# Kernel optimization log

Measured on AMD Instinct MI355X. Metric: run time of the kernel, lower is better.

## Reference

```python
import jax, jax.numpy as jnp
import numpy as np

# Block sizes: 3-hop sampled bipartite graphs (src -> dst per layer)
N_SRC0, N_DST0, E0 = 500_000, 100_000, 1_000_000
N_DST1, E1 = 10_000, 100_000
N_DST2, E2 = 1_024, 10_240
D_IN, D_HID, N_CLS = 128, 128, 47


def setup_inputs() -> dict:
    key = jax.random.key(0)
    ks = jax.random.split(key, 16)
    feats = jax.random.normal(ks[0], (N_SRC0, D_IN), dtype=jnp.float32)
    src0 = jax.random.randint(ks[1], (E0,), 0, N_SRC0)
    dst0 = jax.random.randint(ks[2], (E0,), 0, N_DST0)
    src1 = jax.random.randint(ks[3], (E1,), 0, N_DST0)
    dst1 = jax.random.randint(ks[4], (E1,), 0, N_DST1)
    src2 = jax.random.randint(ks[5], (E2,), 0, N_DST1)
    dst2 = jax.random.randint(ks[6], (E2,), 0, N_DST2)
    # fsi.inverse_idx reindex + NPFeatureShuffle all-to-all -> two permutations
    inverse_idx = jax.random.permutation(ks[7], N_DST0)
    shuffle_idx = jax.random.permutation(ks[8], N_DST0)
    def glorot(k, fan_in, fan_out):
        lim = np.sqrt(6.0 / (fan_in + fan_out)).astype(np.float32)
        return jax.random.uniform(k, (fan_in, fan_out), jnp.float32, -lim, lim)
    W0 = glorot(ks[9], D_IN, D_HID)
    b0 = jnp.zeros((D_HID,), jnp.float32)
    W1 = glorot(ks[10], D_HID, D_HID)
    b1 = jnp.zeros((D_HID,), jnp.float32)
    W2 = glorot(ks[11], D_HID, N_CLS)
    b2 = jnp.zeros((N_CLS,), jnp.float32)
    return dict(feats=feats, src0=src0, dst0=dst0, src1=src1, dst1=dst1,
                src2=src2, dst2=dst2, inverse_idx=inverse_idx,
                shuffle_idx=shuffle_idx, W0=W0, b0=b0, W1=W1, b1=b1, W2=W2, b2=b2)


def _graph_conv(h_src, src, dst, n_src, n_dst, W, b, norm_both):
    # DGL GraphConv: optional D^{-1/2} on src, W, sum-aggregate over edges,
    # optional D^{-1/2} on dst, + bias. Degrees clamped to min 1.
    ones = jnp.ones(src.shape[0], dtype=h_src.dtype)
    if norm_both:
        out_deg = jax.ops.segment_sum(ones, src, num_segments=n_src)
        h_src = h_src * jax.lax.rsqrt(jnp.clip(out_deg, 1.0, None))[:, None]
    msgs = (h_src @ W)[src]                      # [E, d_out] gather
    agg = jax.ops.segment_sum(msgs, dst, num_segments=n_dst)  # scatter-add
    if norm_both:
        in_deg = jax.ops.segment_sum(ones, dst, num_segments=n_dst)
        agg = agg * jax.lax.rsqrt(jnp.clip(in_deg, 1.0, None))[:, None]
    return agg + b


def reference(feats, src0, dst0, src1, dst1, src2, dst2,
              inverse_idx, shuffle_idx, W0, b0, W1, b1, W2, b2):
    # layer 0: norm='none'
    h = _graph_conv(feats, src0, dst0, N_SRC0, N_DST0, W0, b0, norm_both=False)
    # fsi.inverse_idx reindex + NPFeatureShuffle (modeled as permutations)
    h = h[inverse_idx]
    h = h[shuffle_idx]
    h = jax.nn.relu(h)  # dropout is identity in eval
    # layer 1: norm='both'
    h = _graph_conv(h, src1, dst1, N_DST0, N_DST1, W1, b1, norm_both=True)
    h = jax.nn.relu(h)
    # layer 2: norm='both'
    h = _graph_conv(h, src2, dst2, N_DST1, N_DST2, W2, b2, norm_both=True)
    return h
```

## Files before the change

kernel.cpp:

```cpp
#include <hip/hip_runtime.h>
#include <stdint.h>

typedef unsigned int u32;
typedef unsigned short u16;
typedef __attribute__((ext_vector_type(8))) short short8;
typedef __attribute__((ext_vector_type(4))) float f32x4;

#define N_SRC0 500000
#define N_DST0 100000
#define N_DST1 10000
#define N_DST2 1024
#define NCLS 47

#define NB0 98
#define NB1 10
#define NB2 1
#define NBLK 109

static __device__ __forceinline__ float bf16_lo(u32 v) { return __uint_as_float(v << 16); }
static __device__ __forceinline__ float bf16_hi(u32 v) { return __uint_as_float(v & 0xffff0000u); }
static __device__ __forceinline__ float bf16_to_f(u16 s) { return __uint_as_float(((u32)s) << 16); }
static __device__ __forceinline__ u16 f_to_bf16(float f) {
    u32 u = __float_as_uint(f);
    u32 r = u + 0x7fffu + ((u >> 16) & 1u);
    return (u16)(r >> 16);
}

#define OFF_X1     0u
#define OFF_X2     51200000u
#define OFF_CSR0   56320000u
#define OFF_CSR1   60320000u
#define OFF_CSR2   60720000u
#define OFF_RS0    60760960u
#define OFF_CUR0   61160976u
#define OFF_RS1    61560976u
#define OFF_CUR1   61600992u
#define OFF_RS2    61640992u
#define OFF_CUR2   61645104u
#define OFF_CNT0   61649200u
#define OFF_DS1    62049200u
#define OFF_DD1    62449200u
#define OFF_DS2    62489200u
#define OFF_DD2    62529200u
#define ZERO_OFF   OFF_CNT0
#define ZERO_N4    55256u
#define OFF_WF0    62533296u
#define OFF_WF1    62598832u
#define OFF_WC2    62664368u
#define OFF_BC0    62688432u
#define OFF_BC1    62688944u
#define OFF_BC2    62689456u
#define OFF_FLAG   62689712u
#define OFF_BSUM   62689776u
#define OFF_BOFF   62690224u

__global__ __launch_bounds__(256) void k_prep(
    const u32* __restrict__ feats_w,
    const void* __restrict__ W0, const void* __restrict__ b0,
    const void* __restrict__ W1, const void* __restrict__ b1,
    const void* __restrict__ W2, const void* __restrict__ b2,
    float4* __restrict__ zbase,
    u16* __restrict__ wf0, u16* __restrict__ wf1,
    float* __restrict__ wc2, float* __restrict__ bc0,
    float* __restrict__ bc1, float* __restrict__ bc2,
    u32* __restrict__ flag)
{
    int b = blockIdx.x, t = threadIdx.x;
    if (b < 216) {
        u32 i = b * 256 + t;
        if (i < ZERO_N4) zbase[i] = make_float4(0.f, 0.f, 0.f, 0.f);
        return;
    }
    if (b == 216) {
        if (t < 64) {
            u32 u = feats_w[t];
            int e = (u >> 23) & 0xff;
            unsigned long long m = __ballot(e >= 0xC0);
            if (t == 0) *flag = (m != 0ull) ? 1u : 0u;
        }
        return;
    }
    __shared__ u32 lflag;
    if (b < 233) {
        const void* W = (b < 225) ? W0 : W1;
        u16* dst = (b < 225) ? wf0 : wf1;
        int base = ((b < 225) ? (b - 217) : (b - 225)) * 256;
        if (t == 0) lflag = 0u;
        __syncthreads();
        if (t < 64) { u32 u = ((const u32*)W)[t]; if (((u >> 23) & 0xff) >= 0xC0) atomicOr(&lflag, 1u); }
        __syncthreads();
        bool bf = (lflag != 0u);
        int idx = base + t;
        int fid = idx >> 6, lane = idx & 63;
        int nt = fid >> 2, ks = fid & 3;
        #pragma unroll
        for (int j = 0; j < 8; ++j) {
            int k = ks * 32 + (lane >> 4) * 8 + j;
            int n = nt * 16 + (lane & 15);
            u16 v = bf ? ((const u16*)W)[k * 128 + n]
                       : f_to_bf16(((const float*)W)[k * 128 + n]);
            dst[idx * 8 + j] = v;
        }
        return;
    }
    if (b < 257) {
        if (t == 0) lflag = 0u;
        __syncthreads();
        if (t < 64) { u32 u = ((const u32*)W2)[t]; if (((u >> 23) & 0xff) >= 0xC0) atomicOr(&lflag, 1u); }
        __syncthreads();
        bool bf = (lflag != 0u);
        int i = (b - 233) * 256 + t;
        if (i < 128 * NCLS)
            wc2[i] = bf ? bf16_to_f(((const u16*)W2)[i]) : ((const float*)W2)[i];
        return;
    }
    if (t < 128) { bc0[t] = ((const float*)b0)[t]; bc1[t] = ((const float*)b1)[t]; }
    if (t < NCLS) bc2[t] = ((const float*)b2)[t];
}

__global__ __launch_bounds__(256) void k_deg_all(
    const int* __restrict__ dst0,
    const int* __restrict__ src1, const int* __restrict__ dst1,
    const int* __restrict__ src2, const int* __restrict__ dst2,
    u32* __restrict__ cnt0, u32* __restrict__ dS1, u32* __restrict__ dD1,
    u32* __restrict__ dS2, u32* __restrict__ dD2, int E0, int E1, int E2)
{
    int i = blockIdx.x * 256 + threadIdx.x;
    if (i < E0) atomicAdd(&cnt0[dst0[i]], 1u);
    if (i < E1) { atomicAdd(&dS1[src1[i]], 1u); atomicAdd(&dD1[dst1[i]], 1u); }
    if (i < E2) { atomicAdd(&dS2[src2[i]], 1u); atomicAdd(&dD2[dst2[i]], 1u); }
}

static __device__ __forceinline__ void seg_map(int b, const u32* cnt0, const u32* dD1,
                                               const u32* dD2, const u32*& cnt,
                                               int& base, int& n, int& seg) {
    if (b < NB0)            { cnt = cnt0; base = b * 1024;          n = N_DST0; seg = 0; }
    else if (b < NB0 + NB1) { cnt = dD1;  base = (b - NB0) * 1024;  n = N_DST1; seg = 1; }
    else                    { cnt = dD2;  base = 0;                 n = N_DST2; seg = 2; }
}

__global__ __launch_bounds__(256) void k_bsum(
    const u32* __restrict__ cnt0, const u32* __restrict__ dD1,
    const u32* __restrict__ dD2, u32* __restrict__ bsum)
{
    const u32* cnt; int base, n, seg;
    seg_map(blockIdx.x, cnt0, dD1, dD2, cnt, base, n, seg);
    int t = threadIdx.x;
    int i0 = base + t * 4;
    u32 s = 0;
    #pragma unroll
    for (int j = 0; j < 4; ++j) { int i = i0 + j; if (i < n) s += cnt[i]; }
    #pragma unroll
    for (int off = 32; off; off >>= 1) s += __shfl_down(s, off, 64);
    __shared__ u32 wsum[4];
    if ((t & 63) == 0) wsum[t >> 6] = s;
    __syncthreads();
    if (t == 0) bsum[blockIdx.x] = wsum[0] + wsum[1] + wsum[2] + wsum[3];
}

__global__ void k_bscan(const u32* __restrict__ bsum, u32* __restrict__ boff,
                        u32* __restrict__ rs0, u32* __restrict__ rs1,
                        u32* __restrict__ rs2)
{
    if (threadIdx.x != 0) return;
    u32 run = 0;
    for (int b = 0; b < NB0; ++b) { boff[b] = run; run += bsum[b]; }
    rs0[N_DST0] = run;
    run = 0;
    for (int b = NB0; b < NB0 + NB1; ++b) { boff[b] = run; run += bsum[b]; }
    rs1[N_DST1] = run;
    boff[NB0 + NB1] = 0;
    rs2[N_DST2] = bsum[NB0 + NB1];
}

__global__ __launch_bounds__(256) void k_bwrite(
    const u32* __restrict__ cnt0, const u32* __restrict__ dD1,
    const u32* __restrict__ dD2, const u32* __restrict__ boff,
    u32* __restrict__ rs0, u32* __restrict__ cur0,
    u32* __restrict__ rs1, u32* __restrict__ cur1,
    u32* __restrict__ rs2, u32* __restrict__ cur2)
{
    const u32* cnt; int base, n, seg;
    seg_map(blockIdx.x, cnt0, dD1, dD2, cnt, base, n, seg);
    u32 *rs, *cur;
    if (seg == 0)      { rs = rs0; cur = cur0; }
    else if (seg == 1) { rs = rs1; cur = cur1; }
    else               { rs = rs2; cur = cur2; }

    int t = threadIdx.x;
    int i0 = base + t * 4;
    u32 c[4]; u32 s = 0;
    #pragma unroll
    for (int j = 0; j < 4; ++j) {
        int i = i0 + j;
        c[j] = (i < n) ? cnt[i] : 0u;
        s += c[j];
    }
    __shared__ u32 sc[256];
    sc[t] = s;
    __syncthreads();
    #pragma unroll
    for (int off = 1; off < 256; off <<= 1) {
        u32 v = (t >= off) ? sc[t - off] : 0u;
        __syncthreads();
        sc[t] += v;
        __syncthreads();
    }
    u32 ex = sc[t] - s + boff[blockIdx.x];
    #pragma unroll
    for (int j = 0; j < 4; ++j) {
        int i = i0 + j;
        if (i < n) { rs[i] = ex; cur[i] = ex; ex += c[j]; }
    }
}

__global__ __launch_bounds__(256) void k_fill(
    const int* __restrict__ src0, const int* __restrict__ dst0,
    const int* __restrict__ src1, const int* __restrict__ dst1,
    const int* __restrict__ src2, const int* __restrict__ dst2,
    u32* __restrict__ cur0, int* __restrict__ csr0,
    u32* __restrict__ cur1, int* __restrict__ csr1,
    u32* __restrict__ cur2, int* __restrict__ csr2,
    int E0, int E1, int E2)
{
    int i = blockIdx.x * 256 + threadIdx.x;
    if (i < E0) { u32 p = atomicAdd(&cur0[dst0[i]], 1u); csr0[p] = src0[i]; }
    if (i < E1) { u32 p = atomicAdd(&cur1[dst1[i]], 1u); csr1[p] = src1[i]; }
    if (i < E2) { u32 p = atomicAdd(&cur2[dst2[i]], 1u); csr2[p] = src2[i]; }
}

__global__ __launch_bounds__(256) void k_layer(
    const void* __restrict__ Ain, const u32* __restrict__ flag,
    const u32* __restrict__ rs, const int* __restrict__ csr,
    const int* __restrict__ inv, const int* __restrict__ shuf,
    const u32* __restrict__ preDeg, const u32* __restrict__ postDeg,
    const u16* __restrict__ Wfrag, const float* __restrict__ bias,
    float* __restrict__ out, int rows)
{
    __shared__ u16  As[48][136];
    __shared__ u32  eS[48], endS[48];
    __shared__ float preS[48], postS[48], bS[128];

    int tid = threadIdx.x;
    int wv = tid >> 6, lane = tid & 63;
    int I0 = blockIdx.x * 48;

    if (tid < 48) {
        int I = I0 + tid;
        u32 e0 = 0u, e1 = 0u; float pre = 1.f, post = 1.f;
        if (I < rows) {
            int ar = shuf ? inv[shuf[I]] : I;
            e0 = rs[ar]; e1 = rs[ar + 1];
            if (preDeg)  { u32 d = preDeg[I];  pre  = rsqrtf((float)(d > 1u ? d : 1u)); }
            if (postDeg) { u32 d = postDeg[I]; post = rsqrtf((float)(d > 1u ? d : 1u)); }
        }
        eS[tid] = e0; endS[tid] = e1; preS[tid] = pre; postS[tid] = post;
    }
    if (tid < 128) bS[tid] = bias[tid];

    short8 bf[2][4];
    #pragma unroll
    for (int nt = 0; nt < 2; ++nt)
        #pragma unroll
        for (int ks = 0; ks < 4; ++ks) {
            int fid = (wv * 2 + nt) * 4 + ks;
            bf[nt][ks] = *(const short8*)(Wfrag + (size_t)(fid * 64 + lane) * 8);
        }
    __syncthreads();

    bool bfp = flag && (*flag != 0u);
    for (int i = 0; i < 12; ++i) {
        int r = wv * 12 + i;
        u32 e = eS[r], end = endS[r];
        float x = 0.f, y = 0.f;
        if (bfp) {
            const u32* f = (const u32*)Ain;
            for (; e + 8 <= end; e += 8) {
                int s0 = csr[e],   s1 = csr[e+1], s2 = csr[e+2], s3 = csr[e+3];
                int s4 = csr[e+4], s5 = csr[e+5], s6 = csr[e+6], s7 = csr[e+7];
                u32 v0 = f[(size_t)s0 * 64 + lane];
                u32 v1 = f[(size_t)s1 * 64 + lane];
                u32 v2 = f[(size_t)s2 * 64 + lane];
                u32 v3 = f[(size_t)s3 * 64 + lane];
                u32 v4 = f[(size_t)s4 * 64 + lane];
                u32 v5 = f[(size_t)s5 * 64 + lane];
                u32 v6 = f[(size_t)s6 * 64 + lane];
                u32 v7 = f[(size_t)s7 * 64 + lane];
                x += bf16_lo(v0) + bf16_lo(v1) + bf16_lo(v2) + bf16_lo(v3)
                   + bf16_lo(v4) + bf16_lo(v5) + bf16_lo(v6) + bf16_lo(v7);
                y += bf16_hi(v0) + bf16_hi(v1) + bf16_hi(v2) + bf16_hi(v3)
                   + bf16_hi(v4) + bf16_hi(v5) + bf16_hi(v6) + bf16_hi(v7);
            }
            for (; e + 4 <= end; e += 4) {
                int s0 = csr[e], s1 = csr[e+1], s2 = csr[e+2], s3 = csr[e+3];
                u32 v0 = f[(size_t)s0 * 64 + lane];
                u32 v1 = f[(size_t)s1 * 64 + lane];
                u32 v2 = f[(size_t)s2 * 64 + lane];
                u32 v3 = f[(size_t)s3 * 64 + lane];
                x += bf16_lo(v0) + bf16_lo(v1) + bf16_lo(v2) + bf16_lo(v3);
                y += bf16_hi(v0) + bf16_hi(v1) + bf16_hi(v2) + bf16_hi(v3);
            }
            for (; e < end; ++e) {
                u32 v = f[(size_t)csr[e] * 64 + lane];
                x += bf16_lo(v); y += bf16_hi(v);
            }
        } else {
            const float2* f = (const float2*)Ain;
            for (; e + 8 <= end; e += 8) {
                int s0 = csr[e],   s1 = csr[e+1], s2 = csr[e+2], s3 = csr[e+3];
                int s4 = csr[e+4], s5 = csr[e+5], s6 = csr[e+6], s7 = csr[e+7];
                float2 v0 = f[(size_t)s0 * 64 + lane];
                float2 v1 = f[(size_t)s1 * 64 + lane];
                float2 v2 = f[(size_t)s2 * 64 + lane];
                float2 v3 = f[(size_t)s3 * 64 + lane];
                float2 v4 = f[(size_t)s4 * 64 + lane];
                float2 v5 = f[(size_t)s5 * 64 + lane];
                float2 v6 = f[(size_t)s6 * 64 + lane];
                float2 v7 = f[(size_t)s7 * 64 + lane];
                x += v0.x + v1.x + v2.x + v3.x + v4.x + v5.x + v6.x + v7.x;
                y += v0.y + v1.y + v2.y + v3.y + v4.y + v5.y + v6.y + v7.y;
            }
            for (; e + 4 <= end; e += 4) {
                int s0 = csr[e], s1 = csr[e+1], s2 = csr[e+2], s3 = csr[e+3];
                float2 v0 = f[(size_t)s0 * 64 + lane];
                float2 v1 = f[(size_t)s1 * 64 + lane];
                float2 v2 = f[(size_t)s2 * 64 + lane];
                float2 v3 = f[(size_t)s3 * 64 + lane];
                x += v0.x + v1.x + v2.x + v3.x;
                y += v0.y + v1.y + v2.y + v3.y;
            }
            for (; e < end; ++e) {
                float2 v = f[(size_t)csr[e] * 64 + lane];
                x += v.x; y += v.y;
            }
        }
        u32 pk = ((u32)f_to_bf16(y) << 16) | (u32)f_to_bf16(x);
        *(u32*)&As[r][2 * lane] = pk;
    }
    __syncthreads();

    f32x4 acc[2][3];
    #pragma unroll
    for (int nt = 0; nt < 2; ++nt)
        #pragma unroll
        for (int mt = 0; mt < 3; ++mt) acc[nt][mt] = (f32x4){0.f, 0.f, 0.f, 0.f};

    #pragma unroll
    for (int ks = 0; ks < 4; ++ks) {
        short8 af[3];
        #pragma unroll
        for (int mt = 0; mt < 3; ++mt) {
            int row = mt * 16 + (lane & 15);
            int k0 = ks * 32 + (lane >> 4) * 8;
            af[mt] = *(const short8*)&As[row][k0];
        }
        #pragma unroll
        for (int nt = 0; nt < 2; ++nt)
            #pragma unroll
            for (int mt = 0; mt < 3; ++mt)
                acc[nt][mt] = __builtin_amdgcn_mfma_f32_16x16x32_bf16(
                    af[mt], bf[nt][ks], acc[nt][mt], 0, 0, 0);
    }

    int quad = lane >> 4, cl = lane & 15;
    #pragma unroll
    for (int nt = 0; nt < 2; ++nt) {
        int col = (wv * 2 + nt) * 16 + cl;
        float bb = bS[col];
        #pragma unroll
        for (int mt = 0; mt < 3; ++mt) {
            #pragma unroll
            for (int rg = 0; rg < 4; ++rg) {
                int lr = mt * 16 + quad * 4 + rg;
                int I = I0 + lr;
                if (I < rows) {
                    float v = acc[nt][mt][rg] * preS[lr] + bb;
                    v = v > 0.f ? v : 0.f;
                    out[(size_t)I * 128 + col] = v * postS[lr];
                }
            }
        }
    }
}

__global__ __launch_bounds__(256) void k_layer2(
    const float2* __restrict__ x2, const u32* __restrict__ rs,
    const int* __restrict__ csr, const u32* __restrict__ preDeg,
    const float* __restrict__ Wc2, const float* __restrict__ bc2,
    void* __restrict__ out, const u32* __restrict__ flag)
{
    __shared__ float t2[16][128];
    int tid = threadIdx.x;
    int wv = tid >> 6, lane = tid & 63;
    int R0 = blockIdx.x * 16;

    for (int i = 0; i < 4; ++i) {
        int r = wv * 4 + i;
        int R = R0 + r;
        float x = 0.f, y = 0.f;
        u32 e = rs[R], end = rs[R + 1];
        for (; e + 4 <= end; e += 4) {
            int s0 = csr[e], s1 = csr[e+1], s2 = csr[e+2], s3 = csr[e+3];
            float2 v0 = x2[(size_t)s0 * 64 + lane];
            float2 v1 = x2[(size_t)s1 * 64 + lane];
            float2 v2 = x2[(size_t)s2 * 64 + lane];
            float2 v3 = x2[(size_t)s3 * 64 + lane];
            x += v0.x + v1.x + v2.x + v3.x;
            y += v0.y + v1.y + v2.y + v3.y;
        }
        for (; e < end; ++e) {
            float2 v = x2[(size_t)csr[e] * 64 + lane];
            x += v.x; y += v.y;
        }
        t2[r][2 * lane] = x;
        t2[r][2 * lane + 1] = y;
    }
    __syncthreads();

    bool bfp = flag && (*flag != 0u);
    for (int idx = tid; idx < 16 * NCLS; idx += 256) {
        int r = idx / NCLS, c = idx - NCLS * r;
        float a = 0.f;
        #pragma unroll 8
        for (int k = 0; k < 128; ++k) a = fmaf(t2[r][k], Wc2[k * NCLS + c], a);
        u32 d = preDeg[R0 + r];
        float v = a * rsqrtf((float)(d > 1u ? d : 1u)) + bc2[c];
        int g = (R0 + r) * NCLS + c;
        if (bfp) ((u16*)out)[g] = f_to_bf16(v);
        else     ((float*)out)[g] = v;
    }
}

extern "C" void kernel_launch(void* const* d_in, const int* in_sizes, int n_in,
                              void* d_out, int out_size, void* d_ws, size_t ws_size,
                              hipStream_t stream)
{
    (void)n_in; (void)out_size; (void)ws_size;
    const void* feats = d_in[0];
    const int* src0 = (const int*)d_in[1];
    const int* dst0 = (const int*)d_in[2];
    const int* src1 = (const int*)d_in[3];
    const int* dst1 = (const int*)d_in[4];
    const int* src2 = (const int*)d_in[5];
    const int* dst2 = (const int*)d_in[6];
    const int* inv  = (const int*)d_in[7];
    const int* shuf = (const int*)d_in[8];
    const void* W0 = d_in[9];  const void* b0 = d_in[10];
    const void* W1 = d_in[11]; const void* b1 = d_in[12];
    const void* W2 = d_in[13]; const void* b2 = d_in[14];
    int E0 = in_sizes[1], E1 = in_sizes[3], E2 = in_sizes[5];

    char* ws = (char*)d_ws;
    float* x1  = (float*)(ws + OFF_X1);
    float* x2  = (float*)(ws + OFF_X2);
    int* csr0 = (int*)(ws + OFF_CSR0);
    int* csr1 = (int*)(ws + OFF_CSR1);
    int* csr2 = (int*)(ws + OFF_CSR2);
    u32* rs0  = (u32*)(ws + OFF_RS0);
    u32* cur0 = (u32*)(ws + OFF_CUR0);
    u32* rs1  = (u32*)(ws + OFF_RS1);
    u32* cur1 = (u32*)(ws + OFF_CUR1);
    u32* rs2  = (u32*)(ws + OFF_RS2);
    u32* cur2 = (u32*)(ws + OFF_CUR2);
    u32* cnt0 = (u32*)(ws + OFF_CNT0);
    u32* dS1  = (u32*)(ws + OFF_DS1);
    u32* dD1  = (u32*)(ws + OFF_DD1);
    u32* dS2  = (u32*)(ws + OFF_DS2);
    u32* dD2  = (u32*)(ws + OFF_DD2);
    u16* wf0  = (u16*)(ws + OFF_WF0);
    u16* wf1  = (u16*)(ws + OFF_WF1);
    float* wc2 = (float*)(ws + OFF_WC2);
    float* bc0 = (float*)(ws + OFF_BC0);
    float* bc1 = (float*)(ws + OFF_BC1);
    float* bc2 = (float*)(ws + OFF_BC2);
    u32* flag  = (u32*)(ws + OFF_FLAG);
    u32* bsum  = (u32*)(ws + OFF_BSUM);
    u32* boff  = (u32*)(ws + OFF_BOFF);

    k_prep<<<258, 256, 0, stream>>>((const u32*)feats, W0, b0, W1, b1, W2, b2,
                                    (float4*)(ws + ZERO_OFF), wf0, wf1, wc2,
                                    bc0, bc1, bc2, flag);
    k_deg_all<<<(E0 + 255) / 256, 256, 0, stream>>>(dst0, src1, dst1, src2, dst2,
                                                    cnt0, dS1, dD1, dS2, dD2, E0, E1, E2);
    k_bsum<<<NBLK, 256, 0, stream>>>(cnt0, dD1, dD2, bsum);
    k_bscan<<<1, 64, 0, stream>>>(bsum, boff, rs0, rs1, rs2);
    k_bwrite<<<NBLK, 256, 0, stream>>>(cnt0, dD1, dD2, boff,
                                       rs0, cur0, rs1, cur1, rs2, cur2);
    k_fill<<<(E0 + 255) / 256, 256, 0, stream>>>(src0, dst0, src1, dst1, src2, dst2,
                                                 cur0, csr0, cur1, csr1, cur2, csr2,
                                                 E0, E1, E2);
    k_layer<<<(N_DST0 + 47) / 48, 256, 0, stream>>>(
        feats, flag, rs0, csr0, inv, shuf, nullptr, dS1, wf0, bc0, x1, N_DST0);
    k_layer<<<(N_DST1 + 47) / 48, 256, 0, stream>>>(
        x1, nullptr, rs1, csr1, nullptr, nullptr, dD1, dS2, wf1, bc1, x2, N_DST1);
    k_layer2<<<N_DST2 / 16, 256, 0, stream>>>(
        (const float2*)x2, rs2, csr2, dD2, wc2, bc2, d_out, flag);
}
```

Before: 647.2 us.

## Split each wave into two half-waves gathering rows with wider loads and prefetched indices

The layer kernel's gather now has each 64-lane wave handle two destination rows at once, 32 lanes per row, using 8- or 16-byte vector loads instead of 4- or 8-byte ones. Up to 32 neighbor indices per row are loaded cooperatively once and broadcast with shuffles, instead of every lane reading each CSR index. The aim is more memory-level parallelism and fewer redundant index loads in the latency-bound random gather. In exchange there is more shuffle work, divergence when the paired rows have different degrees, and a serial fallback loop for rows with more than 32 neighbors.

```diff
diff --git a/kernel.cpp b/kernel.cpp
--- a/kernel.cpp
+++ b/kernel.cpp
@@ -243,6 +243,7 @@
 
     int tid = threadIdx.x;
     int wv = tid >> 6, lane = tid & 63;
+    int sub = lane >> 5, sl = lane & 31;
     int I0 = blockIdx.x * 48;
 
     if (tid < 48) {
@@ -257,86 +258,101 @@
         eS[tid] = e0; endS[tid] = e1; preS[tid] = pre; postS[tid] = post;
     }
     if (tid < 128) bS[tid] = bias[tid];
-
-    short8 bf[2][4];
+    __syncthreads();
+
+    bool bfp = flag && (*flag != 0u);
+
+    u32 eP[6]; int dgP[6]; int idxP[6];
+    #pragma unroll
+    for (int p = 0; p < 6; ++p) {
+        int rr = wv * 12 + 2 * p + sub;
+        u32 e = eS[rr];
+        int dg = (int)(endS[rr] - e);
+        eP[p] = e; dgP[p] = dg;
+        int mi = 0;
+        if (sl < dg) mi = csr[e + sl];
+        idxP[p] = mi;
+    }
+
+    if (bfp) {
+        const uint2* F = (const uint2*)Ain;
+        #pragma unroll
+        for (int p = 0; p < 6; ++p) {
+            int deg  = dgP[p];
+            int degO = __shfl_xor(deg, 32, 64);
+            int dmax = deg > degO ? deg : degO;
+            int dm32 = dmax < 32 ? dmax : 32;
+            int dg32 = deg  < 32 ? deg  : 32;
+            float x = 0.f, y = 0.f, z = 0.f, w = 0.f;
+            for (int k = 0; k < dm32; k += 4) {
+                int i0 = __shfl(idxP[p], k + 0, 32);
+                int i1 = __shfl(idxP[p], k + 1, 32);
+                int i2 = __shfl(idxP[p], k + 2, 32);
+                int i3 = __shfl(idxP[p], k + 3, 32);
+                uint2 v0 = make_uint2(0u, 0u), v1 = v0, v2 = v0, v3 = v0;
+                if (k + 0 < dg32) v0 = F[(size_t)i0 * 32 + sl];
+                if (k + 1 < dg32) v1 = F[(size_t)i1 * 32 + sl];
+                if (k + 2 < dg32) v2 = F[(size_t)i2 * 32 + sl];
+                if (k + 3 < dg32) v3 = F[(size_t)i3 * 32 + sl];
+                x += bf16_lo(v0.x) + bf16_lo(v1.x) + bf16_lo(v2.x) + bf16_lo(v3.x);
+                y += bf16_hi(v0.x) + bf16_hi(v1.x) + bf16_hi(v2.x) + bf16_hi(v3.x);
+                z += bf16_lo(v0.y) + bf16_lo(v1.y) + bf16_lo(v2.y) + bf16_lo(v3.y);
+                w += bf16_hi(v0.y) + bf16_hi(v1.y) + bf16_hi(v2.y) + bf16_hi(v3.y);
+            }
+            for (int k = 32; k < deg; ++k) {
+                uint2 v = F[(size_t)csr[eP[p] + k] * 32 + sl];
+                x += bf16_lo(v.x); y += bf16_hi(v.x);
+                z += bf16_lo(v.y); w += bf16_hi(v.y);
+            }
+            int rr = wv * 12 + 2 * p + sub;
+            u32 pk0 = ((u32)f_to_bf16(y) << 16) | (u32)f_to_bf16(x);
+            u32 pk1 = ((u32)f_to_bf16(w) << 16) | (u32)f_to_bf16(z);
+            *(uint2*)&As[rr][4 * sl] = make_uint2(pk0, pk1);
+        }
+    } else {
+        const float4* F = (const float4*)Ain;
+        #pragma unroll
+        for (int p = 0; p < 6; ++p) {
+            int deg  = dgP[p];
+            int degO = __shfl_xor(deg, 32, 64);
+            int dmax = deg > degO ? deg : degO;
+            int dm32 = dmax < 32 ? dmax : 32;
+            int dg32 = deg  < 32 ? deg  : 32;
+            float x = 0.f, y = 0.f, z = 0.f, w = 0.f;
+            for (int k = 0; k < dm32; k += 4) {
+                int i0 = __shfl(idxP[p], k + 0, 32);
+                int i1 = __shfl(idxP[p], k + 1, 32);
+                int i2 = __shfl(idxP[p], k + 2, 32);
+                int i3 = __shfl(idxP[p], k + 3, 32);
+                float4 v0 = make_float4(0.f, 0.f, 0.f, 0.f), v1 = v0, v2 = v0, v3 = v0;
+                if (k + 0 < dg32) v0 = F[(size_t)i0 * 32 + sl];
+                if (k + 1 < dg32) v1 = F[(size_t)i1 * 32 + sl];
+                if (k + 2 < dg32) v2 = F[(size_t)i2 * 32 + sl];
+                if (k + 3 < dg32) v3 = F[(size_t)i3 * 32 + sl];
+                x += v0.x + v1.x + v2.x + v3.x;
+                y += v0.y + v1.y + v2.y + v3.y;
+                z += v0.z + v1.z + v2.z + v3.z;
+                w += v0.w + v1.w + v2.w + v3.w;
+            }
+            for (int k = 32; k < deg; ++k) {
+                float4 v = F[(size_t)csr[eP[p] + k] * 32 + sl];
+                x += v.x; y += v.y; z += v.z; w += v.w;
+            }
+            int rr = wv * 12 + 2 * p + sub;
+            u32 pk0 = ((u32)f_to_bf16(y) << 16) | (u32)f_to_bf16(x);
+            u32 pk1 = ((u32)f_to_bf16(w) << 16) | (u32)f_to_bf16(z);
+            *(uint2*)&As[rr][4 * sl] = make_uint2(pk0, pk1);
+        }
+    }
+
+    short8 bfr[2][4];
     #pragma unroll
     for (int nt = 0; nt < 2; ++nt)
         #pragma unroll
         for (int ks = 0; ks < 4; ++ks) {
             int fid = (wv * 2 + nt) * 4 + ks;
-            bf[nt][ks] = *(const short8*)(Wfrag + (size_t)(fid * 64 + lane) * 8);
-        }
-    __syncthreads();
-
-    bool bfp = flag && (*flag != 0u);
-    for (int i = 0; i < 12; ++i) {
-        int r = wv * 12 + i;
-        u32 e = eS[r], end = endS[r];
-        float x = 0.f, y = 0.f;
-        if (bfp) {
-            const u32* f = (const u32*)Ain;
-            for (; e + 8 <= end; e += 8) {
-                int s0 = csr[e],   s1 = csr[e+1], s2 = csr[e+2], s3 = csr[e+3];
-                int s4 = csr[e+4], s5 = csr[e+5], s6 = csr[e+6], s7 = csr[e+7];
-                u32 v0 = f[(size_t)s0 * 64 + lane];
-                u32 v1 = f[(size_t)s1 * 64 + lane];
-                u32 v2 = f[(size_t)s2 * 64 + lane];
-                u32 v3 = f[(size_t)s3 * 64 + lane];
-                u32 v4 = f[(size_t)s4 * 64 + lane];
-                u32 v5 = f[(size_t)s5 * 64 + lane];
-                u32 v6 = f[(size_t)s6 * 64 + lane];
-                u32 v7 = f[(size_t)s7 * 64 + lane];
-                x += bf16_lo(v0) + bf16_lo(v1) + bf16_lo(v2) + bf16_lo(v3)
-                   + bf16_lo(v4) + bf16_lo(v5) + bf16_lo(v6) + bf16_lo(v7);
-                y += bf16_hi(v0) + bf16_hi(v1) + bf16_hi(v2) + bf16_hi(v3)
-                   + bf16_hi(v4) + bf16_hi(v5) + bf16_hi(v6) + bf16_hi(v7);
-            }
-            for (; e + 4 <= end; e += 4) {
-                int s0 = csr[e], s1 = csr[e+1], s2 = csr[e+2], s3 = csr[e+3];
-                u32 v0 = f[(size_t)s0 * 64 + lane];
-                u32 v1 = f[(size_t)s1 * 64 + lane];
-                u32 v2 = f[(size_t)s2 * 64 + lane];
-                u32 v3 = f[(size_t)s3 * 64 + lane];
-                x += bf16_lo(v0) + bf16_lo(v1) + bf16_lo(v2) + bf16_lo(v3);
-                y += bf16_hi(v0) + bf16_hi(v1) + bf16_hi(v2) + bf16_hi(v3);
-            }
-            for (; e < end; ++e) {
-                u32 v = f[(size_t)csr[e] * 64 + lane];
-                x += bf16_lo(v); y += bf16_hi(v);
-            }
-        } else {
-            const float2* f = (const float2*)Ain;
-            for (; e + 8 <= end; e += 8) {
-                int s0 = csr[e],   s1 = csr[e+1], s2 = csr[e+2], s3 = csr[e+3];
-                int s4 = csr[e+4], s5 = csr[e+5], s6 = csr[e+6], s7 = csr[e+7];
-                float2 v0 = f[(size_t)s0 * 64 + lane];
-                float2 v1 = f[(size_t)s1 * 64 + lane];
-                float2 v2 = f[(size_t)s2 * 64 + lane];
-                float2 v3 = f[(size_t)s3 * 64 + lane];
-                float2 v4 = f[(size_t)s4 * 64 + lane];
-                float2 v5 = f[(size_t)s5 * 64 + lane];
-                float2 v6 = f[(size_t)s6 * 64 + lane];
-                float2 v7 = f[(size_t)s7 * 64 + lane];
-                x += v0.x + v1.x + v2.x + v3.x + v4.x + v5.x + v6.x + v7.x;
-                y += v0.y + v1.y + v2.y + v3.y + v4.y + v5.y + v6.y + v7.y;
-            }
-            for (; e + 4 <= end; e += 4) {
-                int s0 = csr[e], s1 = csr[e+1], s2 = csr[e+2], s3 = csr[e+3];
-                float2 v0 = f[(size_t)s0 * 64 + lane];
-                float2 v1 = f[(size_t)s1 * 64 + lane];
-                float2 v2 = f[(size_t)s2 * 64 + lane];
-                float2 v3 = f[(size_t)s3 * 64 + lane];
-                x += v0.x + v1.x + v2.x + v3.x;
-                y += v0.y + v1.y + v2.y + v3.y;
-            }
-            for (; e < end; ++e) {
-                float2 v = f[(size_t)csr[e] * 64 + lane];
-                x += v.x; y += v.y;
-            }
-        }
-        u32 pk = ((u32)f_to_bf16(y) << 16) | (u32)f_to_bf16(x);
-        *(u32*)&As[r][2 * lane] = pk;
-    }
+            bfr[nt][ks] = *(const short8*)(Wfrag + (size_t)(fid * 64 + lane) * 8);
+        }
     __syncthreads();
 
     f32x4 acc[2][3];
@@ -359,7 +375,7 @@
             #pragma unroll
             for (int mt = 0; mt < 3; ++mt)
                 acc[nt][mt] = __builtin_amdgcn_mfma_f32_16x16x32_bf16(
-                    af[mt], bf[nt][ks], acc[nt][mt], 0, 0, 0);
+                    af[mt], bfr[nt][ks], acc[nt][mt], 0, 0, 0);
     }
 
     int quad = lane >> 4, cl = lane & 15;
```

After: 646.9 us. Within noise of the previous version (-0.0%).

## Balance edge gather across waves via flattened edge list and LDS atomics

Applied to the files above, without the earlier changes.

Instead of each wave walking the neighbour lists of 12 fixed rows, the block builds a prefix sum of row degrees, flattens its edges into a shared-memory list of packed (row, src) pairs, and splits that edge range evenly across the four waves. Each wave gathers source features and accumulates into a float LDS tile with atomic adds, using a lane-dependent column swizzle to reduce bank conflicts, then converts the tile to bf16 for the MFMA step. This targets the load imbalance caused by uneven degrees, at the cost of LDS atomics, extra shared memory that may lower occupancy, and a binary-search fallback when a block has more than 1536 edges.

```diff
diff --git a/kernel.cpp b/kernel.cpp
--- a/kernel.cpp
+++ b/kernel.cpp
@@ -16,6 +16,8 @@
 #define NB1 10
 #define NB2 1
 #define NBLK 109
+
+#define ECAP 1536
 
 static __device__ __forceinline__ float bf16_lo(u32 v) { return __uint_as_float(v << 16); }
 static __device__ __forceinline__ float bf16_hi(u32 v) { return __uint_as_float(v & 0xffff0000u); }
@@ -237,13 +239,18 @@
     const u16* __restrict__ Wfrag, const float* __restrict__ bias,
     float* __restrict__ out, int rows)
 {
-    __shared__ u16  As[48][136];
-    __shared__ u32  eS[48], endS[48];
+    __shared__ __align__(16) float Af[48][128];
+    __shared__ __align__(16) u16   As[48][136];
+    __shared__ __align__(16) u32   listS[ECAP];
+    __shared__ u32  eBaseS[48], degS[48], offsS[49];
     __shared__ float preS[48], postS[48], bS[128];
 
     int tid = threadIdx.x;
     int wv = tid >> 6, lane = tid & 63;
     int I0 = blockIdx.x * 48;
+
+    for (int i = tid; i < 48 * 32; i += 256)
+        ((float4*)Af)[i] = make_float4(0.f, 0.f, 0.f, 0.f);
 
     if (tid < 48) {
         int I = I0 + tid;
@@ -254,89 +261,153 @@
             if (preDeg)  { u32 d = preDeg[I];  pre  = rsqrtf((float)(d > 1u ? d : 1u)); }
             if (postDeg) { u32 d = postDeg[I]; post = rsqrtf((float)(d > 1u ? d : 1u)); }
         }
-        eS[tid] = e0; endS[tid] = e1; preS[tid] = pre; postS[tid] = post;
+        eBaseS[tid] = e0; degS[tid] = e1 - e0;
+        preS[tid] = pre; postS[tid] = post;
     }
     if (tid < 128) bS[tid] = bias[tid];
-
-    short8 bf[2][4];
+    __syncthreads();
+
+    if (tid < 64) {
+        u32 d = (tid < 48) ? degS[tid] : 0u;
+        u32 inc = d;
+        #pragma unroll
+        for (int off = 1; off < 64; off <<= 1) {
+            u32 o = __shfl_up(inc, off, 64);
+            if (tid >= off) inc += o;
+        }
+        if (tid < 48) offsS[tid + 1] = inc;
+        if (tid == 0) offsS[0] = 0u;
+    }
+    __syncthreads();
+
+    int totE = (int)offsS[48];
+
+    for (int j = tid; j < totE && j < ECAP; j += 256) {
+        int lo = 0, hi = 47;
+        #pragma unroll
+        for (int it = 0; it < 6; ++it) {
+            int mid = (lo + hi + 1) >> 1;
+            bool ge = ((int)offsS[mid] <= j);
+            lo = ge ? mid : lo;
+            hi = ge ? hi : mid - 1;
+        }
+        u32 src = (u32)csr[eBaseS[lo] + (u32)(j - (int)offsS[lo])];
+        listS[j] = ((u32)lo << 20) | (src & 0xFFFFFu);
+    }
+    __syncthreads();
+
+    bool bfp = flag && (*flag != 0u);
+
+    int per = (((totE + 3) >> 2) + 7) & ~7;
+    int jb = wv * per;
+    int je = jb + per; if (je > totE) je = totE;
+
+    int q  = (lane >> 4) & 1;
+    int cA = (2 * lane) ^ q;
+    int cB = cA ^ 1;
+
+    if (bfp) {
+        const u32* F = (const u32*)Ain;
+        for (int j = jb; j < je; j += 8) {
+            if (j + 8 <= je && j + 8 <= ECAP) {
+                uint4 a = *(const uint4*)&listS[j];
+                uint4 b = *(const uint4*)&listS[j + 4];
+                u32 pk[8] = {a.x, a.y, a.z, a.w, b.x, b.y, b.z, b.w};
+                u32 v[8]; int rr[8];
+                #pragma unroll
+                for (int u = 0; u < 8; ++u) {
+                    rr[u] = (int)(pk[u] >> 20);
+                    v[u] = F[(size_t)(pk[u] & 0xFFFFFu) * 64 + lane];
+                }
+                #pragma unroll
+                for (int u = 0; u < 8; ++u) {
+                    float vx = bf16_lo(v[u]), vy = bf16_hi(v[u]);
+                    atomicAdd(&Af[rr[u]][cA], q ? vy : vx);
+                    atomicAdd(&Af[rr[u]][cB], q ? vx : vy);
+                }
+            } else {
+                for (int u = 0; u < 8; ++u) {
+                    int jj = j + u;
+                    if (jj >= je) break;
+                    int r; u32 src;
+                    if (jj < ECAP) { u32 p = listS[jj]; r = (int)(p >> 20); src = p & 0xFFFFFu; }
+                    else {
+                        int lo = 0, hi = 47;
+                        #pragma unroll
+                        for (int it = 0; it < 6; ++it) {
+                            int mid = (lo + hi + 1) >> 1;
+                            bool ge = ((int)offsS[mid] <= jj);
+                            lo = ge ? mid : lo;
+                            hi = ge ? hi : mid - 1;
+                        }
+                        r = lo; src = (u32)csr[eBaseS[lo] + (u32)(jj - (int)offsS[lo])];
+                    }
+                    u32 vv = F[(size_t)src * 64 + lane];
+                    float vx = bf16_lo(vv), vy = bf16_hi(vv);
+                    atomicAdd(&Af[r][cA], q ? vy : vx);
+                    atomicAdd(&Af[r][cB], q ? vx : vy);
+                }
+            }
+        }
+    } else {
+        const float2* F = (const float2*)Ain;
+        for (int j = jb; j < je; j += 8) {
+            if (j + 8 <= je && j + 8 <= ECAP) {
+                uint4 a = *(const uint4*)&listS[j];
+                uint4 b = *(const uint4*)&listS[j + 4];
+                u32 pk[8] = {a.x, a.y, a.z, a.w, b.x, b.y, b.z, b.w};
+                float2 v[8]; int rr[8];
+                #pragma unroll
+                for (int u = 0; u < 8; ++u) {
+                    rr[u] = (int)(pk[u] >> 20);
+                    v[u] = F[(size_t)(pk[u] & 0xFFFFFu) * 64 + lane];
+                }
+                #pragma unroll
+                for (int u = 0; u < 8; ++u) {
+                    float vx = v[u].x, vy = v[u].y;
+                    atomicAdd(&Af[rr[u]][cA], q ? vy : vx);
+                    atomicAdd(&Af[rr[u]][cB], q ? vx : vy);
+                }
+            } else {
+                for (int u = 0; u < 8; ++u) {
+                    int jj = j + u;
+                    if (jj >= je) break;
+                    int r; u32 src;
+                    if (jj < ECAP) { u32 p = listS[jj]; r = (int)(p >> 20); src = p & 0xFFFFFu; }
+                    else {
+                        int lo = 0, hi = 47;
+                        #pragma unroll
+                        for (int it = 0; it < 6; ++it) {
+                            int mid = (lo + hi + 1) >> 1;
+                            bool ge = ((int)offsS[mid] <= jj);
+                            lo = ge ? mid : lo;
+                            hi = ge ? hi : mid - 1;
+                        }
+                        r = lo; src = (u32)csr[eBaseS[lo] + (u32)(jj - (int)offsS[lo])];
+                    }
+                    float2 vv = F[(size_t)src * 64 + lane];
+                    atomicAdd(&Af[r][cA], q ? vv.y : vv.x);
+                    atomicAdd(&Af[r][cB], q ? vv.x : vv.y);
+                }
+            }
+        }
+    }
+    __syncthreads();
+
+    for (int i = tid; i < 48 * 64; i += 256) {
+        int r = i >> 6, c2 = (i & 63) * 2;
+        u32 pk2 = ((u32)f_to_bf16(Af[r][c2 + 1]) << 16) | (u32)f_to_bf16(Af[r][c2]);
+        *(u32*)&As[r][c2] = pk2;
+    }
+
+    short8 bfr[2][4];
     #pragma unroll
     for (int nt = 0; nt < 2; ++nt)
         #pragma unroll
         for (int ks = 0; ks < 4; ++ks) {
             int fid = (wv * 2 + nt) * 4 + ks;
-            bf[nt][ks] = *(const short8*)(Wfrag + (size_t)(fid * 64 + lane) * 8);
-        }
-    __syncthreads();
-
-    bool bfp = flag && (*flag != 0u);
-    for (int i = 0; i < 12; ++i) {
-        int r = wv * 12 + i;
-        u32 e = eS[r], end = endS[r];
-        float x = 0.f, y = 0.f;
-        if (bfp) {
-            const u32* f = (const u32*)Ain;
-            for (; e + 8 <= end; e += 8) {
-                int s0 = csr[e],   s1 = csr[e+1], s2 = csr[e+2], s3 = csr[e+3];
-                int s4 = csr[e+4], s5 = csr[e+5], s6 = csr[e+6], s7 = csr[e+7];
-                u32 v0 = f[(size_t)s0 * 64 + lane];
-                u32 v1 = f[(size_t)s1 * 64 + lane];
-                u32 v2 = f[(size_t)s2 * 64 + lane];
-                u32 v3 = f[(size_t)s3 * 64 + lane];
-                u32 v4 = f[(size_t)s4 * 64 + lane];
-                u32 v5 = f[(size_t)s5 * 64 + lane];
-                u32 v6 = f[(size_t)s6 * 64 + lane];
-                u32 v7 = f[(size_t)s7 * 64 + lane];
-                x += bf16_lo(v0) + bf16_lo(v1) + bf16_lo(v2) + bf16_lo(v3)
-                   + bf16_lo(v4) + bf16_lo(v5) + bf16_lo(v6) + bf16_lo(v7);
-                y += bf16_hi(v0) + bf16_hi(v1) + bf16_hi(v2) + bf16_hi(v3)
-                   + bf16_hi(v4) + bf16_hi(v5) + bf16_hi(v6) + bf16_hi(v7);
-            }
-            for (; e + 4 <= end; e += 4) {
-                int s0 = csr[e], s1 = csr[e+1], s2 = csr[e+2], s3 = csr[e+3];
-                u32 v0 = f[(size_t)s0 * 64 + lane];
-                u32 v1 = f[(size_t)s1 * 64 + lane];
-                u32 v2 = f[(size_t)s2 * 64 + lane];
-                u32 v3 = f[(size_t)s3 * 64 + lane];
-                x += bf16_lo(v0) + bf16_lo(v1) + bf16_lo(v2) + bf16_lo(v3);
-                y += bf16_hi(v0) + bf16_hi(v1) + bf16_hi(v2) + bf16_hi(v3);
-            }
-            for (; e < end; ++e) {
-                u32 v = f[(size_t)csr[e] * 64 + lane];
-                x += bf16_lo(v); y += bf16_hi(v);
-            }
-        } else {
-            const float2* f = (const float2*)Ain;
-            for (; e + 8 <= end; e += 8) {
-                int s0 = csr[e],   s1 = csr[e+1], s2 = csr[e+2], s3 = csr[e+3];
-                int s4 = csr[e+4], s5 = csr[e+5], s6 = csr[e+6], s7 = csr[e+7];
-                float2 v0 = f[(size_t)s0 * 64 + lane];
-                float2 v1 = f[(size_t)s1 * 64 + lane];
-                float2 v2 = f[(size_t)s2 * 64 + lane];
-                float2 v3 = f[(size_t)s3 * 64 + lane];
-                float2 v4 = f[(size_t)s4 * 64 + lane];
-                float2 v5 = f[(size_t)s5 * 64 + lane];
-                float2 v6 = f[(size_t)s6 * 64 + lane];
-                float2 v7 = f[(size_t)s7 * 64 + lane];
-                x += v0.x + v1.x + v2.x + v3.x + v4.x + v5.x + v6.x + v7.x;
-                y += v0.y + v1.y + v2.y + v3.y + v4.y + v5.y + v6.y + v7.y;
-            }
-            for (; e + 4 <= end; e += 4) {
-                int s0 = csr[e], s1 = csr[e+1], s2 = csr[e+2], s3 = csr[e+3];
-                float2 v0 = f[(size_t)s0 * 64 + lane];
-                float2 v1 = f[(size_t)s1 * 64 + lane];
-                float2 v2 = f[(size_t)s2 * 64 + lane];
-                float2 v3 = f[(size_t)s3 * 64 + lane];
-                x += v0.x + v1.x + v2.x + v3.x;
-                y += v0.y + v1.y + v2.y + v3.y;
-            }
-            for (; e < end; ++e) {
-                float2 v = f[(size_t)csr[e] * 64 + lane];
-                x += v.x; y += v.y;
-            }
-        }
-        u32 pk = ((u32)f_to_bf16(y) << 16) | (u32)f_to_bf16(x);
-        *(u32*)&As[r][2 * lane] = pk;
-    }
+            bfr[nt][ks] = *(const short8*)(Wfrag + (size_t)(fid * 64 + lane) * 8);
+        }
     __syncthreads();
 
     f32x4 acc[2][3];
@@ -359,7 +430,7 @@
             #pragma unroll
             for (int mt = 0; mt < 3; ++mt)
                 acc[nt][mt] = __builtin_amdgcn_mfma_f32_16x16x32_bf16(
-                    af[mt], bf[nt][ks], acc[nt][mt], 0, 0, 0);
+                    af[mt], bfr[nt][ks], acc[nt][mt], 0, 0, 0);
     }
 
     int quad = lane >> 4, cl = lane & 15;
```

Measured after the change: 1.277 ms. +97.4%, slower.
